# Performance work log

Measured on AMD Instinct MI355X. Metric: run time of the kernel, lower is better.

The kernel has to match this reference:

```python
import jax, jax.numpy as jnp
import numpy as np

LAMBDA_COORD = 5.0
LAMBDA_NOOBJ = 0.5
EPS = 1e-9


def _bbox_iou(px, py, pr, gx, gy, gr):
    """IoU of the axis-aligned bounding squares of two circles (x, y, r)."""
    l1, r1, t1, b1 = px - pr, px + pr, py - pr, py + pr
    l2, r2, t2, b2 = gx - gr, gx + gr, gy - gr, gy + gr
    iw = jnp.maximum(jnp.minimum(r1, r2) - jnp.maximum(l1, l2), 0.0)
    ih = jnp.maximum(jnp.minimum(b1, b2) - jnp.maximum(t1, t2), 0.0)
    inter = iw * ih
    a1 = (r1 - l1) * (b1 - t1)
    a2 = (r2 - l2) * (b2 - t2)
    return inter / (a1 + a2 - inter + EPS)


def setup_inputs() -> dict:
    key = jax.random.key(0)
    k1, k2, k3, k4 = jax.random.split(key, 4)
    B, L, G, C = 65536, 16, 8, 8
    pred = jax.random.uniform(k1, (B, G, G, C), dtype=jnp.float32)
    label_rc = jax.random.randint(k2, (B, L, 2), 0, G, dtype=jnp.int32)
    xy = jax.random.uniform(k3, (B, L, 2), dtype=jnp.float32)
    r = jax.random.uniform(k4, (B, L, 1), dtype=jnp.float32) * 0.2 + 0.01
    label_box = jnp.concatenate([xy, r], axis=-1)
    return {"pred": pred, "label_rc": label_rc, "label_box": label_box}


def reference(pred, label_rc, label_box):
    B = pred.shape[0]
    rows = label_rc[..., 0]  # [B, L]
    cols = label_rc[..., 1]
    bidx = jnp.arange(B)[:, None]
    pb = pred[bidx, rows, cols]  # [B, L, 8] responsible cell per label

    gx, gy, gr = label_box[..., 0], label_box[..., 1], label_box[..., 2]
    iou1 = _bbox_iou(pb[..., 0], pb[..., 1], pb[..., 2], gx, gy, gr)
    iou2 = _bbox_iou(pb[..., 4], pb[..., 5], pb[..., 6], gx, gy, gr)

    swap = iou2 > iou1
    cx = jnp.where(swap, pb[..., 4], pb[..., 0])
    cy = jnp.where(swap, pb[..., 5], pb[..., 1])
    cr = jnp.where(swap, pb[..., 6], pb[..., 2])
    conf = jnp.where(swap, pb[..., 7], pb[..., 3])
    un_conf = jnp.where(swap, pb[..., 3], pb[..., 7])
    bigger = jnp.where(swap, iou2, iou1)
    smaller = jnp.where(swap, iou1, iou2)

    coord_loss = LAMBDA_COORD * jnp.sum(
        (cx - gx) ** 2 + (cy - gy) ** 2 + (cr - gr) ** 2)
    cond_loss = jnp.sum((bigger - conf) ** 2)
    cond_loss = cond_loss + LAMBDA_NOOBJ * jnp.sum((smaller - un_conf) ** 2)

    # object mask over the 8x8 grid (duplicates collapse to 1, as in original)
    obj_mask = jnp.zeros(pred.shape[:3], dtype=pred.dtype).at[bidx, rows, cols].set(1.0)
    noobj = (pred[..., 3] ** 2 + pred[..., 7] ** 2) * (1.0 - obj_mask)
    cond_loss = cond_loss + LAMBDA_NOOBJ * jnp.sum(noobj)

    return (coord_loss + cond_loss) / B
```

## Files before the change

kernel.cpp:

```cpp
#include <hip/hip_runtime.h>


static constexpr float LAMBDA_COORD = 5.0f;
static constexpr float LAMBDA_NOOBJ = 0.5f;
static constexpr float EPS_F = 1e-9f;

#define WAVES_PER_BLOCK 4
#define SUPER  4
#define SUPERS 2

__device__ __forceinline__ float bbox_iou(float px, float py, float pr,
                                          float gx, float gy, float gr) {
    float l1 = px - pr, r1 = px + pr, t1 = py - pr, b1 = py + pr;
    float l2 = gx - gr, r2 = gx + gr, t2 = gy - gr, b2 = gy + gr;
    float iw = fmaxf(fminf(r1, r2) - fmaxf(l1, l2), 0.0f);
    float ih = fmaxf(fminf(b1, b2) - fmaxf(t1, t2), 0.0f);
    float inter = iw * ih;
    float a1 = (r1 - l1) * (b1 - t1);
    float a2 = (r2 - l2) * (b2 - t2);
    return inter / (a1 + a2 - inter + EPS_F);
}

#define LOAD_SUPER(dst, b0)                                                    \
    {                                                                          \
        _Pragma("unroll")                                                      \
        for (int q = 0; q < SUPER; ++q) {                                      \
            const long b_ = (b0) + q;                                          \
            if (b_ < (long)B) {                                                \
                const float4* gp_ = (const float4*)(pred + b_ * 512);          \
                dst[2 * q]     = gp_[lane];                                    \
                dst[2 * q + 1] = gp_[lane + 64];                               \
            } else {                                                           \
                dst[2 * q]     = make_float4(0.f, 0.f, 0.f, 0.f);              \
                dst[2 * q + 1] = make_float4(0.f, 0.f, 0.f, 0.f);              \
            }                                                                  \
        }                                                                      \
    }

#define PROC_SUPER(buf, b0)                                                    \
    {                                                                          \
                            \
        if (lane < SUPER * 2) my_mask[lane] = 0u;                              \
        _Pragma("unroll")                                                      \
        for (int q = 0; q < SUPER; ++q) {                                      \
            noobj_acc += buf[2 * q].w     * buf[2 * q].w                       \
                       + buf[2 * q + 1].w * buf[2 * q + 1].w;                  \
            float4* sp4_ = (float4*)(my_stage + q * 512);                      \
            sp4_[lane]      = buf[2 * q];                                      \
            sp4_[lane + 64] = buf[2 * q + 1];                                  \
        }                                                                      \
        asm volatile("s_waitcnt lgkmcnt(0)" ::: "memory");                     \
        const long bq_ = (b0) + grp;                                           \
        if (bq_ < (long)B && lj < L) {                                         \
            const int2 rc_ = *(const int2*)(label_rc + ((size_t)bq_ * L + lj) * 2); \
            const float* lb_ = label_box + ((size_t)bq_ * L + lj) * 3;         \
            const float gx = lb_[0], gy = lb_[1], gr = lb_[2];                 \
            const int cell_ = rc_.x * 8 + rc_.y;                               \
            const float4* cp_ = (const float4*)(my_stage + grp * 512 + cell_ * 8); \
            const float4 c0_ = cp_[0];                                         \
            const float4 c1_ = cp_[1];                                         \
            const unsigned bit_ = 1u << (cell_ & 31);                          \
            const unsigned old_ = atomicOr(&my_mask[grp * 2 + (cell_ >> 5)], bit_); \
            const float p0 = c0_.x, p1 = c0_.y, p2 = c0_.z, p3 = c0_.w;        \
            const float p4 = c1_.x, p5 = c1_.y, p6 = c1_.z, p7 = c1_.w;        \
            const float iou1 = bbox_iou(p0, p1, p2, gx, gy, gr);               \
            const float iou2 = bbox_iou(p4, p5, p6, gx, gy, gr);               \
            const bool  sw_ = iou2 > iou1;                                     \
            const float cx = sw_ ? p4 : p0;                                    \
            const float cy = sw_ ? p5 : p1;                                    \
            const float cr = sw_ ? p6 : p2;                                    \
            const float conf    = sw_ ? p7 : p3;                               \
            const float un_conf = sw_ ? p3 : p7;                               \
            const float bigger  = sw_ ? iou2 : iou1;                           \
            const float smaller = sw_ ? iou1 : iou2;                           \
            const float dx = cx - gx, dy = cy - gy, dr = cr - gr;              \
            main_acc += LAMBDA_COORD * (dx * dx + dy * dy + dr * dr);          \
            const float d1 = bigger - conf;                                    \
            main_acc += d1 * d1;                                               \
            const float d2 = smaller - un_conf;                                \
            noobj_acc += d2 * d2;                                              \
            if ((old_ & bit_) == 0u)         \
                noobj_acc -= (p3 * p3 + p7 * p7);                              \
        }                                                                      \
    }

__global__ __launch_bounds__(256, 4) void yolo_loss_kernel(
    const float* __restrict__ pred,
    const int*   __restrict__ label_rc,
    const float* __restrict__ label_box,
    float* __restrict__ partials,
    int B, int L)
{
    __shared__ float    stage[WAVES_PER_BLOCK][SUPER * 512];
    __shared__ unsigned cmask[WAVES_PER_BLOCK][SUPER * 2];
    __shared__ float    wsum[WAVES_PER_BLOCK];

    const int tid  = threadIdx.x;
    const int lane = tid & 63;
    const int wv   = tid >> 6;
    const int grp  = lane >> 4;
    const int lj   = lane & 15;

    float*    my_stage = stage[wv];
    unsigned* my_mask  = cmask[wv];

    const long b_base =
        ((long)blockIdx.x * WAVES_PER_BLOCK + wv) * (SUPER * SUPERS);

    float main_acc  = 0.0f;
    float noobj_acc = 0.0f;

    float4 bufA[2 * SUPER];
    float4 bufB[2 * SUPER];
    LOAD_SUPER(bufA, b_base);
    LOAD_SUPER(bufB, b_base + SUPER);

    PROC_SUPER(bufA, b_base);
    PROC_SUPER(bufB, b_base + SUPER);

    float acc = main_acc + LAMBDA_NOOBJ * noobj_acc;
    #pragma unroll
    for (int off = 32; off > 0; off >>= 1)
        acc += __shfl_xor(acc, off);
    if (lane == 0) wsum[wv] = acc;
    __syncthreads();
    if (tid == 0)
        partials[blockIdx.x] = wsum[0] + wsum[1] + wsum[2] + wsum[3];
}

__global__ __launch_bounds__(256) void reduce_kernel(
    const float* __restrict__ partials, float* __restrict__ out,
    int n, float invB)
{
    float s = 0.0f;
    for (int i = threadIdx.x; i < n; i += 256)
        s += partials[i];
    #pragma unroll
    for (int off = 32; off > 0; off >>= 1)
        s += __shfl_xor(s, off);

    __shared__ float wsum[4];
    const int lane = threadIdx.x & 63, w = threadIdx.x >> 6;
    if (lane == 0) wsum[w] = s;
    __syncthreads();
    if (threadIdx.x == 0)
        out[0] = (wsum[0] + wsum[1] + wsum[2] + wsum[3]) * invB;
}

extern "C" void kernel_launch(void* const* d_in, const int* in_sizes, int n_in,
                              void* d_out, int out_size, void* d_ws, size_t ws_size,
                              hipStream_t stream) {
    const float* pred      = (const float*)d_in[0];
    const int*   label_rc  = (const int*)d_in[1];
    const float* label_box = (const float*)d_in[2];
    float*       out       = (float*)d_out;
    float*       partials  = (float*)d_ws;

    const int B = in_sizes[0] / 512;
    const int L = in_sizes[1] / (B * 2);
    const float invB = 1.0f / (float)B;

    const int batches_per_block = WAVES_PER_BLOCK * SUPER * SUPERS;
    const int blocks = (B + batches_per_block - 1) / batches_per_block;

    yolo_loss_kernel<<<blocks, 256, 0, stream>>>(
        pred, label_rc, label_box, partials, B, L);

    reduce_kernel<<<1, 256, 0, stream>>>(partials, out, blocks, invB);
}
```

Measured before the change: 206.3 us.

## Use persistent grid with double-buffered loads and drop LDS staging

Switches to a fixed grid of 1024 blocks where each wave loops over a contiguous range of 4-batch super groups, prefetching the next group's pred tile and label data while processing the current one. The LDS staging of pred is removed: the responsible-cell values are re-read from global memory (likely cache hits) instead of from shared memory. This aims to cut launch and tail overhead, shrink shared memory use and overlap memory latency with compute. In exchange each wave holds two register buffers and does dependent global gathers.

Measured after the change: 209.6 us. About the same (+1.6%).

```diff
diff --git a/kernel.cpp b/kernel.cpp
--- a/kernel.cpp
+++ b/kernel.cpp
@@ -7,7 +7,7 @@
 
 #define WAVES_PER_BLOCK 4
 #define SUPER  4
-#define SUPERS 2
+#define NBLOCKS 1024
 
 __device__ __forceinline__ float bbox_iou(float px, float py, float pr,
                                           float gx, float gy, float gr) {
@@ -21,50 +21,60 @@
     return inter / (a1 + a2 - inter + EPS_F);
 }
 
-#define LOAD_SUPER(dst, b0)                                                    \
+#define DECL_SUPER(S)                                                          \
+    float4 S##_q0, S##_q1, S##_q2, S##_q3, S##_q4, S##_q5, S##_q6, S##_q7;     \
+    int    S##_cell = 0, S##_ok = 0;                                           \
+    float  S##_gx = 0.f, S##_gy = 0.f, S##_gr = 0.f;
+
+#define LOAD_SUPER(S, g)                                                       \
     {                                                                          \
-        _Pragma("unroll")                                                      \
-        for (int q = 0; q < SUPER; ++q) {                                      \
-            const long b_ = (b0) + q;                                          \
-            if (b_ < (long)B) {                                                \
-                const float4* gp_ = (const float4*)(pred + b_ * 512);          \
-                dst[2 * q]     = gp_[lane];                                    \
-                dst[2 * q + 1] = gp_[lane + 64];                               \
-            } else {                                                           \
-                dst[2 * q]     = make_float4(0.f, 0.f, 0.f, 0.f);              \
-                dst[2 * q + 1] = make_float4(0.f, 0.f, 0.f, 0.f);              \
-            }                                                                  \
+        const long bb_ = (long)(g) * SUPER;                                    \
+        const float4* gp_ = (const float4*)(pred + bb_ * 512);                 \
+        if (bb_ + SUPER <= (long)B) {               \
+            S##_q0 = gp_[lane];        S##_q1 = gp_[lane + 64];                \
+            S##_q2 = gp_[lane + 128];  S##_q3 = gp_[lane + 192];               \
+            S##_q4 = gp_[lane + 256];  S##_q5 = gp_[lane + 320];               \
+            S##_q6 = gp_[lane + 384];  S##_q7 = gp_[lane + 448];               \
+        } else {                                                               \
+            const float4 z_ = make_float4(0.f, 0.f, 0.f, 0.f);                 \
+            S##_q0 = S##_q1 = S##_q2 = S##_q3 = z_;                            \
+            S##_q4 = S##_q5 = S##_q6 = S##_q7 = z_;                            \
+            if (bb_ + 0 < (long)B) { S##_q0 = gp_[lane];       S##_q1 = gp_[lane + 64];  } \
+            if (bb_ + 1 < (long)B) { S##_q2 = gp_[lane + 128]; S##_q3 = gp_[lane + 192]; } \
+            if (bb_ + 2 < (long)B) { S##_q4 = gp_[lane + 256]; S##_q5 = gp_[lane + 320]; } \
+            if (bb_ + 3 < (long)B) { S##_q6 = gp_[lane + 384]; S##_q7 = gp_[lane + 448]; } \
+        }                                                                      \
+        const long bq_ = bb_ + grp;                                            \
+        S##_ok = (bq_ < (long)B) && (lj < L);                                  \
+        if (S##_ok) {                                                          \
+            const int2 rc_ = *(const int2*)(label_rc + ((size_t)bq_ * L + lj) * 2); \
+            S##_cell = rc_.x * 8 + rc_.y;                           \
+            const float* lb_ = label_box + ((size_t)bq_ * L + lj) * 3;         \
+            S##_gx = lb_[0]; S##_gy = lb_[1]; S##_gr = lb_[2];                 \
         }                                                                      \
     }
 
-#define PROC_SUPER(buf, b0)                                                    \
+#define PROC_SUPER(S, g)                                                       \
     {                                                                          \
-                            \
+        noobj_acc += S##_q0.w * S##_q0.w + S##_q1.w * S##_q1.w                 \
+                   + S##_q2.w * S##_q2.w + S##_q3.w * S##_q3.w                 \
+                   + S##_q4.w * S##_q4.w + S##_q5.w * S##_q5.w                 \
+                   + S##_q6.w * S##_q6.w + S##_q7.w * S##_q7.w;                \
         if (lane < SUPER * 2) my_mask[lane] = 0u;                              \
-        _Pragma("unroll")                                                      \
-        for (int q = 0; q < SUPER; ++q) {                                      \
-            noobj_acc += buf[2 * q].w     * buf[2 * q].w                       \
-                       + buf[2 * q + 1].w * buf[2 * q + 1].w;                  \
-            float4* sp4_ = (float4*)(my_stage + q * 512);                      \
-            sp4_[lane]      = buf[2 * q];                                      \
-            sp4_[lane + 64] = buf[2 * q + 1];                                  \
-        }                                                                      \
         asm volatile("s_waitcnt lgkmcnt(0)" ::: "memory");                     \
-        const long bq_ = (b0) + grp;                                           \
-        if (bq_ < (long)B && lj < L) {                                         \
-            const int2 rc_ = *(const int2*)(label_rc + ((size_t)bq_ * L + lj) * 2); \
-            const float* lb_ = label_box + ((size_t)bq_ * L + lj) * 3;         \
-            const float gx = lb_[0], gy = lb_[1], gr = lb_[2];                 \
-            const int cell_ = rc_.x * 8 + rc_.y;                               \
-            const float4* cp_ = (const float4*)(my_stage + grp * 512 + cell_ * 8); \
-            const float4 c0_ = cp_[0];                                         \
+        if (S##_ok) {                                                          \
+            const long bq_ = (long)(g) * SUPER + grp;                          \
+            const float4* cp_ =                                                \
+                (const float4*)(pred + (size_t)bq_ * 512 + (size_t)S##_cell * 8); \
+            const float4 c0_ = cp_[0];          \
             const float4 c1_ = cp_[1];                                         \
-            const unsigned bit_ = 1u << (cell_ & 31);                          \
-            const unsigned old_ = atomicOr(&my_mask[grp * 2 + (cell_ >> 5)], bit_); \
+            const unsigned bit_ = 1u << (S##_cell & 31);                       \
+            const unsigned old_ =                                              \
+                atomicOr(&my_mask[grp * 2 + (S##_cell >> 5)], bit_);           \
             const float p0 = c0_.x, p1 = c0_.y, p2 = c0_.z, p3 = c0_.w;        \
             const float p4 = c1_.x, p5 = c1_.y, p6 = c1_.z, p7 = c1_.w;        \
-            const float iou1 = bbox_iou(p0, p1, p2, gx, gy, gr);               \
-            const float iou2 = bbox_iou(p4, p5, p6, gx, gy, gr);               \
+            const float iou1 = bbox_iou(p0, p1, p2, S##_gx, S##_gy, S##_gr);   \
+            const float iou2 = bbox_iou(p4, p5, p6, S##_gx, S##_gy, S##_gr);   \
             const bool  sw_ = iou2 > iou1;                                     \
             const float cx = sw_ ? p4 : p0;                                    \
             const float cy = sw_ ? p5 : p1;                                    \
@@ -73,7 +83,7 @@
             const float un_conf = sw_ ? p3 : p7;                               \
             const float bigger  = sw_ ? iou2 : iou1;                           \
             const float smaller = sw_ ? iou1 : iou2;                           \
-            const float dx = cx - gx, dy = cy - gy, dr = cr - gr;              \
+            const float dx = cx - S##_gx, dy = cy - S##_gy, dr = cr - S##_gr;  \
             main_acc += LAMBDA_COORD * (dx * dx + dy * dy + dr * dr);          \
             const float d1 = bigger - conf;                                    \
             main_acc += d1 * d1;                                               \
@@ -91,7 +101,6 @@
     float* __restrict__ partials,
     int B, int L)
 {
-    __shared__ float    stage[WAVES_PER_BLOCK][SUPER * 512];
     __shared__ unsigned cmask[WAVES_PER_BLOCK][SUPER * 2];
     __shared__ float    wsum[WAVES_PER_BLOCK];
 
@@ -101,22 +110,33 @@
     const int grp  = lane >> 4;
     const int lj   = lane & 15;
 
-    float*    my_stage = stage[wv];
-    unsigned* my_mask  = cmask[wv];
+    unsigned* my_mask = cmask[wv];
 
-    const long b_base =
-        ((long)blockIdx.x * WAVES_PER_BLOCK + wv) * (SUPER * SUPERS);
+    const long waves_tot = (long)gridDim.x * WAVES_PER_BLOCK;
+    const long wgid      = (long)blockIdx.x * WAVES_PER_BLOCK + wv;
+    const long nsup      = ((long)B + SUPER - 1) / SUPER;
+    const long spw       = (nsup + waves_tot - 1) / waves_tot;
+    const long g_begin   = wgid * spw;
+    const long g_end     = (g_begin + spw < nsup) ? (g_begin + spw) : nsup;
 
     float main_acc  = 0.0f;
     float noobj_acc = 0.0f;
 
-    float4 bufA[2 * SUPER];
-    float4 bufB[2 * SUPER];
-    LOAD_SUPER(bufA, b_base);
-    LOAD_SUPER(bufB, b_base + SUPER);
+    DECL_SUPER(A)
+    DECL_SUPER(B)
 
-    PROC_SUPER(bufA, b_base);
-    PROC_SUPER(bufB, b_base + SUPER);
+    long g = g_begin;
+    if (g < g_end) {
+        LOAD_SUPER(A, g);
+        while (true) {
+            if (g + 1 < g_end) LOAD_SUPER(B, g + 1);
+            PROC_SUPER(A, g);
+            ++g; if (g >= g_end) break;
+            if (g + 1 < g_end) LOAD_SUPER(A, g + 1);
+            PROC_SUPER(B, g);
+            ++g; if (g >= g_end) break;
+        }
+    }
 
     float acc = main_acc + LAMBDA_NOOBJ * noobj_acc;
     #pragma unroll
@@ -160,11 +180,8 @@
     const int L = in_sizes[1] / (B * 2);
     const float invB = 1.0f / (float)B;
 
-    const int batches_per_block = WAVES_PER_BLOCK * SUPER * SUPERS;
-    const int blocks = (B + batches_per_block - 1) / batches_per_block;
-
-    yolo_loss_kernel<<<blocks, 256, 0, stream>>>(
+    yolo_loss_kernel<<<NBLOCKS, 256, 0, stream>>>(
         pred, label_rc, label_box, partials, B, L);
 
-    reduce_kernel<<<1, 256, 0, stream>>>(partials, out, blocks, invB);
+    reduce_kernel<<<1, 256, 0, stream>>>(partials, out, NBLOCKS, invB);
 }
```
